# Performance work log

Measured on AMD Instinct MI355X. Metric: run time of the kernel, lower is better.

## Reference

```python
import jax, jax.numpy as jnp
import numpy as np

DIM = 512
NUM_HEADS = 8
HEAD_DIM = DIM // NUM_HEADS
MAX_SLICES = 1024
SCALE = float(np.sqrt(HEAD_DIM))


def setup_inputs() -> dict:
    key = jax.random.key(0)
    ks = jax.random.split(key, 12)
    B, Nv, Nt, D = 4, 1024, 512, DIM
    std = 0.02
    inp = {
        "visual_tokens": jax.random.normal(ks[0], (B, Nv, D), jnp.float32),
        "text_tokens": jax.random.normal(ks[1], (B, Nt, D), jnp.float32),
        # Linear weights stored as [in, out] (i.e., torch W^T), so y = x @ W + b
        "W_Q": jax.random.normal(ks[2], (D, D), jnp.float32) * std,
        "b_Q": jnp.zeros((D,), jnp.float32),
        "W_K": jax.random.normal(ks[3], (D, D), jnp.float32) * std,
        "b_K": jnp.zeros((D,), jnp.float32),
        "W_V": jax.random.normal(ks[4], (D, D), jnp.float32) * std,
        "b_V": jnp.zeros((D,), jnp.float32),
        "W_O": jax.random.normal(ks[5], (D, D), jnp.float32) * std,
        "b_O": jnp.zeros((D,), jnp.float32),
        "bias_table": jax.random.normal(ks[6], (2 * MAX_SLICES - 1, NUM_HEADS), jnp.float32) * std,
        "ln_gamma": jnp.ones((D,), jnp.float32),
        "ln_beta": jnp.zeros((D,), jnp.float32),
    }
    return inp


def _layernorm(x, gamma, beta, eps=1e-5):
    mu = jnp.mean(x, axis=-1, keepdims=True)
    var = jnp.var(x, axis=-1, keepdims=True)
    return (x - mu) * jax.lax.rsqrt(var + eps) * gamma + beta


def reference(visual_tokens, text_tokens, W_Q, b_Q, W_K, b_K, W_V, b_V, W_O, b_O,
              bias_table, ln_gamma, ln_beta):
    Z = jnp.concatenate([visual_tokens, text_tokens], axis=1)  # [B, N, D]
    B, N, D = Z.shape
    Z = _layernorm(Z, ln_gamma, ln_beta)

    def proj(W, b):
        return (Z @ W + b).reshape(B, N, NUM_HEADS, HEAD_DIM).transpose(0, 2, 1, 3)

    Q = proj(W_Q, b_Q)  # [B, H, N, hd]
    K = proj(W_K, b_K)
    V = proj(W_V, b_V)

    attn = jnp.einsum("bhqd,bhkd->bhqk", Q, K) / SCALE  # [B, H, N, N]

    # relative slice bias: [H, N, N]
    coords = jnp.arange(N)
    rel = coords[:, None] - coords[None, :] + (MAX_SLICES - 1)
    rel = jnp.clip(rel, 0, 2 * MAX_SLICES - 2)
    bias = bias_table[rel]                      # [N, N, H]
    bias = jnp.transpose(bias, (2, 0, 1))[None]  # [1, H, N, N]

    attn = jax.nn.softmax(attn + bias, axis=-1)
    out = jnp.einsum("bhqk,bhkd->bhqd", attn, V)  # [B, H, N, hd]
    out = out.transpose(0, 2, 1, 3).reshape(B, N, D)
    return out @ W_O + b_O
```

## Files before the change

kernel.cpp:

```cpp
#include <hip/hip_runtime.h>
#include <stdint.h>

#define NSEQ   1536
#define NBATCH 4
#define NM     (NBATCH * NSEQ)
#define DMODEL 512
#define NHEAD  8
#define HD     64
#define TBLN   2047

typedef __attribute__((ext_vector_type(4))) float  f32x4;
typedef __attribute__((ext_vector_type(4))) int    i32x4;
typedef __attribute__((ext_vector_type(8))) __bf16 bf16x8;
typedef unsigned short u16;

static_assert(sizeof(bf16x8) == 16, "bf16x8 must be 16B");

__device__ inline u16 f2bf(float f) {
  union { float f; uint32_t u; } v; v.f = f;
  uint32_t u = v.u;
  return (u16)((u + 0x7fffu + ((u >> 16) & 1u)) >> 16);
}

__device__ inline bf16x8 ld_bf8(const u16* p) {
  i32x4 v = *(const i32x4*)p;
  return __builtin_bit_cast(bf16x8, v);
}

__device__ inline f32x4 mfma16(bf16x8 a, bf16x8 b, f32x4 c) {
  return __builtin_amdgcn_mfma_f32_16x16x32_bf16(a, b, c, 0, 0, 0);
}

__device__ inline void gload_lds16(const void* g, void* l) {
  __builtin_amdgcn_global_load_lds(
      (__attribute__((address_space(1))) void*)(g),
      (__attribute__((address_space(3))) void*)(l), 16, 0, 0);
}

__device__ inline uint32_t pkbf(float a, float b) {
  uint32_t r;
  asm("v_cvt_pk_bf16_f32 %0, %1, %2" : "=v"(r) : "v"(a), "v"(b));
  return r;
}

__device__ inline float exp2_raw(float x) {
  float r;
  asm("v_exp_f32 %0, %1" : "=v"(r) : "v"(x));
  return r;
}

__global__ __launch_bounds__(256) void ln_kernel(
    const float* __restrict__ vis, const float* __restrict__ txt,
    const float* __restrict__ gamma, const float* __restrict__ beta,
    u16* __restrict__ zn) {
  const int lane = threadIdx.x & 63;
  const int row  = blockIdx.x * 4 + (threadIdx.x >> 6);
  const int b = row / NSEQ, n = row - b * NSEQ;
  const float* src = (n < 1024) ? (vis + ((size_t)b * 1024 + n) * DMODEL)
                                : (txt + ((size_t)b * 512 + (n - 1024)) * DMODEL);
  const float4* s4 = (const float4*)src;
  float4 x0 = s4[lane], x1 = s4[lane + 64];
  float s = x0.x + x0.y + x0.z + x0.w + x1.x + x1.y + x1.z + x1.w;
  float q = x0.x*x0.x + x0.y*x0.y + x0.z*x0.z + x0.w*x0.w
          + x1.x*x1.x + x1.y*x1.y + x1.z*x1.z + x1.w*x1.w;
  #pragma unroll
  for (int m = 1; m < 64; m <<= 1) { s += __shfl_xor(s, m); q += __shfl_xor(q, m); }
  const float mean = s * (1.0f / 512.0f);
  const float var  = q * (1.0f / 512.0f) - mean * mean;
  const float rstd = rsqrtf(var + 1e-5f);
  const float4* g4 = (const float4*)gamma;
  const float4* b4 = (const float4*)beta;
  float4 g0 = g4[lane], g1 = g4[lane + 64], p0 = b4[lane], p1 = b4[lane + 64];
  u16* dst = zn + (size_t)row * DMODEL;
  ushort4 o0, o1;
  o0.x = f2bf((x0.x - mean) * rstd * g0.x + p0.x);
  o0.y = f2bf((x0.y - mean) * rstd * g0.y + p0.y);
  o0.z = f2bf((x0.z - mean) * rstd * g0.z + p0.z);
  o0.w = f2bf((x0.w - mean) * rstd * g0.w + p0.w);
  o1.x = f2bf((x1.x - mean) * rstd * g1.x + p1.x);
  o1.y = f2bf((x1.y - mean) * rstd * g1.y + p1.y);
  o1.z = f2bf((x1.z - mean) * rstd * g1.z + p1.z);
  o1.w = f2bf((x1.w - mean) * rstd * g1.w + p1.w);
  *(ushort4*)(dst + lane * 4)        = o0;
  *(ushort4*)(dst + (lane + 64) * 4) = o1;
}

__global__ __launch_bounds__(256) void wtrans_kernel(
    const float* __restrict__ WQ, const float* __restrict__ WK,
    const float* __restrict__ WV, const float* __restrict__ WO,
    u16* __restrict__ wqkvt, u16* __restrict__ wot) {
  __shared__ float t[32][33];
  const int m = blockIdx.z;
  const float* W = (m == 0) ? WQ : (m == 1) ? WK : (m == 2) ? WV : WO;
  const int n0 = blockIdx.x * 32, k0 = blockIdx.y * 32;
  const int tx = threadIdx.x & 31, ty = threadIdx.x >> 5;
  #pragma unroll
  for (int j = 0; j < 4; ++j)
    t[ty + j * 8][tx] = W[(size_t)(k0 + ty + j * 8) * DMODEL + n0 + tx];
  __syncthreads();
  u16* out = (m < 3) ? (wqkvt + (size_t)m * DMODEL * DMODEL) : wot;
  #pragma unroll
  for (int j = 0; j < 4; ++j)
    out[(size_t)(n0 + ty + j * 8) * DMODEL + k0 + tx] = f2bf(t[tx][ty + j * 8]);
}

__global__ __launch_bounds__(256) void gemm_qkv(
    const u16* __restrict__ A, const u16* __restrict__ Bt,
    const float* __restrict__ bQ, const float* __restrict__ bK, const float* __restrict__ bV,
    u16* __restrict__ Q, u16* __restrict__ Kk, u16* __restrict__ Vt) {
  __shared__ __align__(16) u16 lat[128 * 64];
  __shared__ __align__(16) u16 lbt[96 * 64];
  const int tid = threadIdx.x, lane = tid & 63, w = tid >> 6;
  const int wr = w >> 1, wc = w & 1;
  const int m0 = blockIdx.y * 128, n0 = blockIdx.x * 96;
  f32x4 acc[4][3] = {};
  for (int kt = 0; kt < 8; ++kt) {
    const int k0 = kt * 64;
    #pragma unroll
    for (int i = 0; i < 4; ++i) {
      int ch = tid + 256 * i;
      int row = ch >> 3, pc = ch & 7;
      int kk = k0 + ((pc ^ (row & 7)) << 3);
      gload_lds16(A + (size_t)(m0 + row) * DMODEL + kk, lat + (size_t)ch * 8);
    }
    #pragma unroll
    for (int i = 0; i < 3; ++i) {
      int ch = tid + 256 * i;
      int row = ch >> 3, pc = ch & 7;
      int kk = k0 + ((pc ^ (row & 7)) << 3);
      gload_lds16(Bt + (size_t)(n0 + row) * DMODEL + kk, lbt + (size_t)ch * 8);
    }
    __syncthreads();
    #pragma unroll
    for (int ks = 0; ks < 2; ++ks) {
      bf16x8 af[4], bfr[3];
      const int cc = ks * 4 + (lane >> 4);
      #pragma unroll
      for (int f = 0; f < 4; ++f) {
        int ra = wr * 64 + f * 16 + (lane & 15);
        af[f]  = ld_bf8(lat + ra * 64 + ((cc ^ (ra & 7)) << 3));
      }
      #pragma unroll
      for (int f = 0; f < 3; ++f) {
        int rb = wc * 48 + f * 16 + (lane & 15);
        bfr[f] = ld_bf8(lbt + rb * 64 + ((cc ^ (rb & 7)) << 3));
      }
      #pragma unroll
      for (int fr = 0; fr < 4; ++fr)
        #pragma unroll
        for (int fc = 0; fc < 3; ++fc)
          acc[fr][fc] = mfma16(af[fr], bfr[fc], acc[fr][fc]);
    }
    __syncthreads();
  }
  #pragma unroll
  for (int fr = 0; fr < 4; ++fr) {
    const int mbase = m0 + wr * 64 + fr * 16 + ((lane >> 4) << 2);
    const int b = mbase / NSEQ;
    const int nseq = mbase - b * NSEQ;
    #pragma unroll
    for (int fc = 0; fc < 3; ++fc) {
      const int col = n0 + wc * 48 + fc * 16 + (lane & 15);
      const int which = col >> 9;
      const int cw = col & 511;
      const int h = cw >> 6, d = cw & 63;
      const float bias = (which == 0) ? bQ[cw] : (which == 1) ? bK[cw] : bV[cw];
      if (which < 2) {
        u16* dst = ((which == 0) ? Q : Kk) + ((size_t)(b * NHEAD + h) * NSEQ + nseq) * HD + d;
        #pragma unroll
        for (int r = 0; r < 4; ++r) dst[(size_t)r * HD] = f2bf(acc[fr][fc][r] + bias);
      } else {
        ushort4 pv;
        pv.x = f2bf(acc[fr][fc][0] + bias);
        pv.y = f2bf(acc[fr][fc][1] + bias);
        pv.z = f2bf(acc[fr][fc][2] + bias);
        pv.w = f2bf(acc[fr][fc][3] + bias);
        *(ushort4*)(Vt + ((size_t)(b * NHEAD + h) * HD + d) * NSEQ + nseq) = pv;
      }
    }
  }
}

__global__ __launch_bounds__(256) void gemm_oproj(
    const u16* __restrict__ A, const u16* __restrict__ Bt,
    const float* __restrict__ bO, float* __restrict__ out) {
  __shared__ __align__(16) u16 lat[64 * 64];
  __shared__ __align__(16) u16 lbt[64 * 64];
  const int tid = threadIdx.x, lane = tid & 63, w = tid >> 6;
  const int wr = w >> 1, wc = w & 1;
  const int m0 = blockIdx.y * 64, n0 = blockIdx.x * 64;
  f32x4 acc[2][2] = {};
  for (int kt = 0; kt < 8; ++kt) {
    const int k0 = kt * 64;
    #pragma unroll
    for (int i = 0; i < 2; ++i) {
      int ch = tid + 256 * i;
      int row = ch >> 3, pc = ch & 7;
      int kk = k0 + ((pc ^ (row & 7)) << 3);
      gload_lds16(A  + (size_t)(m0 + row) * DMODEL + kk, lat + (size_t)ch * 8);
      gload_lds16(Bt + (size_t)(n0 + row) * DMODEL + kk, lbt + (size_t)ch * 8);
    }
    __syncthreads();
    #pragma unroll
    for (int ks = 0; ks < 2; ++ks) {
      bf16x8 af[2], bfr[2];
      const int cc = ks * 4 + (lane >> 4);
      #pragma unroll
      for (int f = 0; f < 2; ++f) {
        int ra = wr * 32 + f * 16 + (lane & 15);
        af[f]  = ld_bf8(lat + ra * 64 + ((cc ^ (ra & 7)) << 3));
        int rb = wc * 32 + f * 16 + (lane & 15);
        bfr[f] = ld_bf8(lbt + rb * 64 + ((cc ^ (rb & 7)) << 3));
      }
      #pragma unroll
      for (int fr = 0; fr < 2; ++fr)
        #pragma unroll
        for (int fc = 0; fc < 2; ++fc)
          acc[fr][fc] = mfma16(af[fr], bfr[fc], acc[fr][fc]);
    }
    __syncthreads();
  }
  #pragma unroll
  for (int fr = 0; fr < 2; ++fr) {
    const int mbase = m0 + wr * 32 + fr * 16 + ((lane >> 4) << 2);
    #pragma unroll
    for (int fc = 0; fc < 2; ++fc) {
      const int col = n0 + wc * 32 + fc * 16 + (lane & 15);
      const float bias = bO[col];
      float* dst = out + (size_t)mbase * DMODEL + col;
      #pragma unroll
      for (int r = 0; r < 4; ++r) dst[(size_t)r * DMODEL] = acc[fr][fc][r] + bias;
    }
  }
}

__global__ __launch_bounds__(384, 2) void attn_kernel(
    const u16* __restrict__ Q, const u16* __restrict__ K,
    const u16* __restrict__ Vt, const float* __restrict__ table,
    u16* __restrict__ O) {
  __shared__ float rblds[3072];
  __shared__ __align__(16) u16 kbuf[2][8192];
  __shared__ __align__(16) u16 vbuf[2][8192];
  __shared__ __align__(16) u16 plds[6][4096];
  const int tid = threadIdx.x, lane = tid & 63, w = tid >> 6;
  const int bid = blockIdx.x;
  const int xcd = bid & 7, idx = bid >> 3;
  const int bh  = xcd * 4 + (idx & 3);
  const int qt  = idx >> 2;
  const int h   = bh & (NHEAD - 1);
  for (int t = tid; t < 3072; t += 384) {
    int src = 2558 - t;
    src = src < 0 ? 0 : (src > 2046 ? 2046 : src);
    rblds[t] = table[(size_t)src * NHEAD + h] * 1.4426950408889634f;
  }

  const int lo16 = lane & 15, g = lane >> 4;
  const int q0 = qt * 192 + w * 32;
  const u16* Qb = Q  + (size_t)bh * NSEQ * HD;
  const u16* Kb = K  + (size_t)bh * NSEQ * HD;
  const u16* Vb = Vt + (size_t)bh * HD * NSEQ;

#define STAGE2(buf, k0)                                                        \
  if (tid < 256) {                                                             \
    _Pragma("unroll")                                                          \
    for (int i = 0; i < 4; ++i) {                                              \
      int ch = tid + 256 * i;                                                  \
      int krow = ch >> 3;                                                      \
      int kcol = ((ch ^ krow) & 7) << 3;                                       \
      gload_lds16(Kb + (size_t)((k0) + krow) * HD + kcol, kbuf[buf] + (size_t)ch * 8); \
      int vrow = ch >> 4;                                                      \
      int vcg  = (ch & 8) | ((ch ^ vrow) & 7);                                 \
      gload_lds16(Vb + (size_t)vrow * NSEQ + (k0) + vcg * 8, vbuf[buf] + (size_t)ch * 8); \
    }                                                                          \
  }

  bf16x8 qf[2][2];
  #pragma unroll
  for (int s = 0; s < 2; ++s)
    #pragma unroll
    for (int kd = 0; kd < 2; ++kd)
      qf[s][kd] = ld_bf8(Qb + (size_t)(q0 + s * 16 + lo16) * HD + kd * 32 + g * 8);

  float l_part[2] = {0.f, 0.f};
  f32x4 acc[2][4] = {};

  char* plb = (char*)plds[w];
  const int pswz  = (lo16 & 7) << 4;
  const int wbase = lo16 * 128;
  const int rswz  = lo16 & 7;
  const float* rbp = rblds + (1535 - q0 - lo16 + 4 * g - 16);
  const float c1 = 0.125f * 1.4426950408889634f;

  STAGE2(0, 0);
  __syncthreads();
  int cur = 0;

  for (int kt = 0; kt < 12; ++kt) {
    const int k0 = kt * 128;
    const int nxt = cur ^ 1;
    if (kt < 11) {
      STAGE2(nxt, k0 + 128);
      if (tid < 256) asm volatile("s_waitcnt vmcnt(8)" ::: "memory");
    } else {
      if (tid < 256) asm volatile("s_waitcnt vmcnt(0)" ::: "memory");
    }
    __builtin_amdgcn_s_barrier();
    const u16* kb = kbuf[cur];
    const u16* vb = vbuf[cur];
    #pragma unroll
    for (int hh = 0; hh < 2; ++hh) {
      char* plh = plb + hh * 4096;
      float bvg[5][4];
      #pragma unroll
      for (int j = 0; j < 5; ++j)
        #pragma unroll
        for (int r = 0; r < 4; ++r)
          bvg[j][r] = rbp[k0 + hh * 64 + 16 * j + r];
      f32x4 st[2][4] = {};
      __builtin_amdgcn_s_setprio(1);
      #pragma unroll
      for (int kc = 0; kc < 4; ++kc) {
        const int row = hh * 64 + kc * 16 + lo16;
        const bf16x8 kf0 = ld_bf8(kb + row * 64 + ((g ^ rswz) << 3));
        const bf16x8 kf1 = ld_bf8(kb + row * 64 + (((4 + g) ^ rswz) << 3));
        #pragma unroll
        for (int s = 0; s < 2; ++s) {
          st[s][kc] = mfma16(kf0, qf[s][0], st[s][kc]);
          st[s][kc] = mfma16(kf1, qf[s][1], st[s][kc]);
        }
      }
      __builtin_amdgcn_s_setprio(0);
      #pragma unroll
      for (int s = 0; s < 2; ++s)
        #pragma unroll
        for (int kc = 0; kc < 4; ++kc) {
          #pragma unroll
          for (int r = 0; r < 4; ++r) {
            float p = exp2_raw(__builtin_fmaf(st[s][kc][r], c1, bvg[kc - s + 1][r]));
            st[s][kc][r] = p;
            l_part[s] += p;
          }
          uint2 pr;
          pr.x = pkbf(st[s][kc][0], st[s][kc][1]);
          pr.y = pkbf(st[s][kc][2], st[s][kc][3]);
          *(uint2*)(plh + s * 2048 + wbase + ((kc * 32 + g * 8) ^ pswz)) = pr;
        }
      __builtin_amdgcn_s_setprio(1);
      #pragma unroll
      for (int t = 0; t < 2; ++t) {
        bf16x8 pb[2];
        #pragma unroll
        for (int s = 0; s < 2; ++s)
          pb[s] = ld_bf8((const u16*)(plh + s * 2048 + wbase + ((t * 64 + g * 16) ^ pswz)));
        #pragma unroll
        for (int fc = 0; fc < 4; ++fc) {
          const int row = fc * 16 + lo16;
          const int cl = (hh * 8) | (((t * 4 + g) ^ rswz) & 7);
          const bf16x8 vf = ld_bf8(vb + row * 128 + cl * 8);
          #pragma unroll
          for (int s = 0; s < 2; ++s)
            acc[s][fc] = mfma16(vf, pb[s], acc[s][fc]);
        }
      }
      __builtin_amdgcn_s_setprio(0);
    }
    __builtin_amdgcn_s_barrier();
    cur = nxt;
  }
  const int b = bh >> 3;
  #pragma unroll
  for (int s = 0; s < 2; ++s) {
    float l_r = l_part[s];
    l_r += __shfl_xor(l_r, 16);
    l_r += __shfl_xor(l_r, 32);
    const float inv = 1.0f / l_r;
    u16* orow = O + ((size_t)(b * NSEQ + q0 + s * 16 + lo16)) * DMODEL + h * HD;
    #pragma unroll
    for (int fc = 0; fc < 4; ++fc) {
      uint2 o4;
      o4.x = pkbf(acc[s][fc][0] * inv, acc[s][fc][1] * inv);
      o4.y = pkbf(acc[s][fc][2] * inv, acc[s][fc][3] * inv);
      *(uint2*)(orow + fc * 16 + g * 4) = o4;
    }
  }
#undef STAGE2
}

extern "C" void kernel_launch(void* const* d_in, const int* in_sizes, int n_in,
                              void* d_out, int out_size, void* d_ws, size_t ws_size,
                              hipStream_t stream) {
  const float* vis   = (const float*)d_in[0];
  const float* txt   = (const float*)d_in[1];
  const float* WQ    = (const float*)d_in[2];
  const float* bQ    = (const float*)d_in[3];
  const float* WK    = (const float*)d_in[4];
  const float* bK    = (const float*)d_in[5];
  const float* WV    = (const float*)d_in[6];
  const float* bV    = (const float*)d_in[7];
  const float* WO    = (const float*)d_in[8];
  const float* bO    = (const float*)d_in[9];
  const float* table = (const float*)d_in[10];
  const float* gamma = (const float*)d_in[11];
  const float* beta  = (const float*)d_in[12];
  float* out = (float*)d_out;

  char* p = (char*)d_ws;
  u16* zn    = (u16*)p; p += (size_t)NM * DMODEL * 2;
  u16* wqkvt = (u16*)p; p += (size_t)3 * DMODEL * DMODEL * 2;
  u16* wot   = (u16*)p; p += (size_t)DMODEL * DMODEL * 2;
  u16* q     = (u16*)p; p += (size_t)NM * DMODEL * 2;
  u16* k     = (u16*)p; p += (size_t)NM * DMODEL * 2;
  u16* vt    = (u16*)p; p += (size_t)NM * DMODEL * 2;
  u16* o     = (u16*)p; p += (size_t)NM * DMODEL * 2;

  hipLaunchKernelGGL(ln_kernel, dim3(NM / 4), dim3(256), 0, stream,
                     vis, txt, gamma, beta, zn);
  hipLaunchKernelGGL(wtrans_kernel, dim3(16, 16, 4), dim3(256), 0, stream,
                     WQ, WK, WV, WO, wqkvt, wot);
  hipLaunchKernelGGL(gemm_qkv, dim3(16, 48), dim3(256), 0, stream,
                     zn, wqkvt, bQ, bK, bV, q, k, vt);
  hipLaunchKernelGGL(attn_kernel, dim3(256), dim3(384), 0, stream,
                     q, k, vt, table, o);
  hipLaunchKernelGGL(gemm_oproj, dim3(8, 96), dim3(256), 0, stream,
                     o, wot, bO, out);
}
```

Measured before the change: 85.01 us.

## Restructure attention to 4 waves with 48 query rows each and 64-key tiles

```diff
diff --git a/kernel.cpp b/kernel.cpp
--- a/kernel.cpp
+++ b/kernel.cpp
@@ -47,6 +47,13 @@
   float r;
   asm("v_exp_f32 %0, %1" : "=v"(r) : "v"(x));
   return r;
+}
+
+__device__ inline float bfhi(uint32_t u) {
+  union { uint32_t u; float f; } v; v.u = u & 0xffff0000u; return v.f;
+}
+__device__ inline float bflo(uint32_t u) {
+  union { uint32_t u; float f; } v; v.u = u << 16; return v.f;
 }
 
 __global__ __launch_bounds__(256) void ln_kernel(
@@ -234,142 +241,143 @@
   }
 }
 
-__global__ __launch_bounds__(384, 2) void attn_kernel(
+__global__ __launch_bounds__(256, 2) void attn_kernel(
     const u16* __restrict__ Q, const u16* __restrict__ K,
     const u16* __restrict__ Vt, const float* __restrict__ table,
     u16* __restrict__ O) {
-  __shared__ float rblds[3072];
-  __shared__ __align__(16) u16 kbuf[2][8192];
-  __shared__ __align__(16) u16 vbuf[2][8192];
-  __shared__ __align__(16) u16 plds[6][4096];
+  __shared__ u16 rb2[2][3072];
+  __shared__ __align__(16) u16 kbuf[2][4096];
+  __shared__ __align__(16) u16 vbuf[2][4096];
+  __shared__ __align__(16) u16 plds[4][3][1024];
   const int tid = threadIdx.x, lane = tid & 63, w = tid >> 6;
   const int bid = blockIdx.x;
   const int xcd = bid & 7, idx = bid >> 3;
   const int bh  = xcd * 4 + (idx & 3);
   const int qt  = idx >> 2;
   const int h   = bh & (NHEAD - 1);
-  for (int t = tid; t < 3072; t += 384) {
-    int src = 2558 - t;
+  for (int t = tid; t < 2 * 3072; t += 256) {
+    const int c = (t >= 3072) ? 1 : 0;
+    const int x = t - c * 3072;
+    int src = 2558 - (x + c);
     src = src < 0 ? 0 : (src > 2046 ? 2046 : src);
-    rblds[t] = table[(size_t)src * NHEAD + h] * 1.4426950408889634f;
+    rb2[c][x] = f2bf(table[(size_t)src * NHEAD + h] * 1.4426950408889634f);
   }
 
   const int lo16 = lane & 15, g = lane >> 4;
-  const int q0 = qt * 192 + w * 32;
+  const int q0 = qt * 192 + w * 48;
   const u16* Qb = Q  + (size_t)bh * NSEQ * HD;
   const u16* Kb = K  + (size_t)bh * NSEQ * HD;
   const u16* Vb = Vt + (size_t)bh * HD * NSEQ;
 
-#define STAGE2(buf, k0)                                                        \
-  if (tid < 256) {                                                             \
-    _Pragma("unroll")                                                          \
-    for (int i = 0; i < 4; ++i) {                                              \
-      int ch = tid + 256 * i;                                                  \
-      int krow = ch >> 3;                                                      \
-      int kcol = ((ch ^ krow) & 7) << 3;                                       \
-      gload_lds16(Kb + (size_t)((k0) + krow) * HD + kcol, kbuf[buf] + (size_t)ch * 8); \
-      int vrow = ch >> 4;                                                      \
-      int vcg  = (ch & 8) | ((ch ^ vrow) & 7);                                 \
-      gload_lds16(Vb + (size_t)vrow * NSEQ + (k0) + vcg * 8, vbuf[buf] + (size_t)ch * 8); \
-    }                                                                          \
-  }
-
-  bf16x8 qf[2][2];
-  #pragma unroll
-  for (int s = 0; s < 2; ++s)
+#define STAGE(buf, k0)                                                        \
+  do {                                                                        \
+    _Pragma("unroll")                                                         \
+    for (int i = 0; i < 2; ++i) {                                             \
+      int ch = tid + 256 * i;                                                 \
+      int row = ch >> 3, pc = ch & 7;                                         \
+      int col = (pc ^ (row & 7)) << 3;                                        \
+      gload_lds16(Kb + (size_t)((k0) + row) * HD + col, kbuf[buf] + (size_t)ch * 8); \
+      gload_lds16(Vb + (size_t)row * NSEQ + (k0) + col, vbuf[buf] + (size_t)ch * 8); \
+    }                                                                         \
+  } while (0)
+
+  bf16x8 qf[3][2];
+  #pragma unroll
+  for (int s = 0; s < 3; ++s)
     #pragma unroll
     for (int kd = 0; kd < 2; ++kd)
       qf[s][kd] = ld_bf8(Qb + (size_t)(q0 + s * 16 + lo16) * HD + kd * 32 + g * 8);
 
-  float l_part[2] = {0.f, 0.f};
-  f32x4 acc[2][4] = {};
-
-  char* plb = (char*)plds[w];
+  float l_part[3] = {0.f, 0.f, 0.f};
+  f32x4 acc[3][4] = {};
+
   const int pswz  = (lo16 & 7) << 4;
   const int wbase = lo16 * 128;
   const int rswz  = lo16 & 7;
-  const float* rbp = rblds + (1535 - q0 - lo16 + 4 * g - 16);
+  const int B   = 1535 - q0 - lo16 + 4 * g - 32;
+  const int c2  = B & 1;
+  const int dwb = (B - c2) >> 1;
+  const uint32_t* rbp32 = (const uint32_t*)rb2[c2];
   const float c1 = 0.125f * 1.4426950408889634f;
 
-  STAGE2(0, 0);
+  STAGE(0, 0);
   __syncthreads();
   int cur = 0;
 
-  for (int kt = 0; kt < 12; ++kt) {
-    const int k0 = kt * 128;
+  for (int kt = 0; kt < 24; ++kt) {
+    const int k0 = kt * 64;
     const int nxt = cur ^ 1;
-    if (kt < 11) {
-      STAGE2(nxt, k0 + 128);
-      if (tid < 256) asm volatile("s_waitcnt vmcnt(8)" ::: "memory");
+    if (kt < 23) {
+      STAGE(nxt, k0 + 64);
+      asm volatile("s_waitcnt vmcnt(4)" ::: "memory");
     } else {
-      if (tid < 256) asm volatile("s_waitcnt vmcnt(0)" ::: "memory");
+      asm volatile("s_waitcnt vmcnt(0)" ::: "memory");
     }
     __builtin_amdgcn_s_barrier();
     const u16* kb = kbuf[cur];
     const u16* vb = vbuf[cur];
-    #pragma unroll
-    for (int hh = 0; hh < 2; ++hh) {
-      char* plh = plb + hh * 4096;
-      float bvg[5][4];
-      #pragma unroll
-      for (int j = 0; j < 5; ++j)
+    float bvf[6][4];
+    #pragma unroll
+    for (int j = 0; j < 6; ++j) {
+      const uint32_t u0 = rbp32[dwb + (k0 >> 1) + 8 * j];
+      const uint32_t u1 = rbp32[dwb + (k0 >> 1) + 8 * j + 1];
+      bvf[j][0] = bflo(u0); bvf[j][1] = bfhi(u0);
+      bvf[j][2] = bflo(u1); bvf[j][3] = bfhi(u1);
+    }
+    f32x4 st[3][4] = {};
+    __builtin_amdgcn_s_setprio(1);
+    #pragma unroll
+    for (int kc = 0; kc < 4; ++kc) {
+      const int row = kc * 16 + lo16;
+      const bf16x8 kf0 = ld_bf8(kb + row * 64 + ((g ^ rswz) << 3));
+      const bf16x8 kf1 = ld_bf8(kb + row * 64 + (((4 + g) ^ rswz) << 3));
+      #pragma unroll
+      for (int s = 0; s < 3; ++s) {
+        st[s][kc] = mfma16(kf0, qf[s][0], st[s][kc]);
+        st[s][kc] = mfma16(kf1, qf[s][1], st[s][kc]);
+      }
+    }
+    __builtin_amdgcn_s_setprio(0);
+    #pragma unroll
+    for (int s = 0; s < 3; ++s) {
+      char* plb = (char*)plds[w][s];
+      #pragma unroll
+      for (int kc = 0; kc < 4; ++kc) {
         #pragma unroll
-        for (int r = 0; r < 4; ++r)
-          bvg[j][r] = rbp[k0 + hh * 64 + 16 * j + r];
-      f32x4 st[2][4] = {};
-      __builtin_amdgcn_s_setprio(1);
-      #pragma unroll
-      for (int kc = 0; kc < 4; ++kc) {
-        const int row = hh * 64 + kc * 16 + lo16;
-        const bf16x8 kf0 = ld_bf8(kb + row * 64 + ((g ^ rswz) << 3));
-        const bf16x8 kf1 = ld_bf8(kb + row * 64 + (((4 + g) ^ rswz) << 3));
+        for (int r = 0; r < 4; ++r) {
+          float p = exp2_raw(__builtin_fmaf(st[s][kc][r], c1, bvf[kc - s + 2][r]));
+          st[s][kc][r] = p;
+          l_part[s] += p;
+        }
+        uint2 pr;
+        pr.x = pkbf(st[s][kc][0], st[s][kc][1]);
+        pr.y = pkbf(st[s][kc][2], st[s][kc][3]);
+        *(uint2*)(plb + wbase + ((kc * 32 + g * 8) ^ pswz)) = pr;
+      }
+    }
+    __builtin_amdgcn_s_setprio(1);
+    #pragma unroll
+    for (int t = 0; t < 2; ++t) {
+      bf16x8 pb[3];
+      #pragma unroll
+      for (int s = 0; s < 3; ++s)
+        pb[s] = ld_bf8((const u16*)((char*)plds[w][s] + wbase + ((t * 64 + g * 16) ^ pswz)));
+      #pragma unroll
+      for (int fc = 0; fc < 4; ++fc) {
+        const int row = fc * 16 + lo16;
+        const bf16x8 vf = ld_bf8(vb + row * 64 + (((t * 4 + g) ^ rswz) << 3));
         #pragma unroll
-        for (int s = 0; s < 2; ++s) {
-          st[s][kc] = mfma16(kf0, qf[s][0], st[s][kc]);
-          st[s][kc] = mfma16(kf1, qf[s][1], st[s][kc]);
-        }
-      }
-      __builtin_amdgcn_s_setprio(0);
-      #pragma unroll
-      for (int s = 0; s < 2; ++s)
-        #pragma unroll
-        for (int kc = 0; kc < 4; ++kc) {
-          #pragma unroll
-          for (int r = 0; r < 4; ++r) {
-            float p = exp2_raw(__builtin_fmaf(st[s][kc][r], c1, bvg[kc - s + 1][r]));
-            st[s][kc][r] = p;
-            l_part[s] += p;
-          }
-          uint2 pr;
-          pr.x = pkbf(st[s][kc][0], st[s][kc][1]);
-          pr.y = pkbf(st[s][kc][2], st[s][kc][3]);
-          *(uint2*)(plh + s * 2048 + wbase + ((kc * 32 + g * 8) ^ pswz)) = pr;
-        }
-      __builtin_amdgcn_s_setprio(1);
-      #pragma unroll
-      for (int t = 0; t < 2; ++t) {
-        bf16x8 pb[2];
-        #pragma unroll
-        for (int s = 0; s < 2; ++s)
-          pb[s] = ld_bf8((const u16*)(plh + s * 2048 + wbase + ((t * 64 + g * 16) ^ pswz)));
-        #pragma unroll
-        for (int fc = 0; fc < 4; ++fc) {
-          const int row = fc * 16 + lo16;
-          const int cl = (hh * 8) | (((t * 4 + g) ^ rswz) & 7);
-          const bf16x8 vf = ld_bf8(vb + row * 128 + cl * 8);
-          #pragma unroll
-          for (int s = 0; s < 2; ++s)
-            acc[s][fc] = mfma16(vf, pb[s], acc[s][fc]);
-        }
-      }
-      __builtin_amdgcn_s_setprio(0);
-    }
+        for (int s = 0; s < 3; ++s)
+          acc[s][fc] = mfma16(vf, pb[s], acc[s][fc]);
+      }
+    }
+    __builtin_amdgcn_s_setprio(0);
     __builtin_amdgcn_s_barrier();
     cur = nxt;
   }
   const int b = bh >> 3;
   #pragma unroll
-  for (int s = 0; s < 2; ++s) {
+  for (int s = 0; s < 3; ++s) {
     float l_r = l_part[s];
     l_r += __shfl_xor(l_r, 16);
     l_r += __shfl_xor(l_r, 32);
@@ -383,7 +391,7 @@
       *(uint2*)(orow + fc * 16 + g * 4) = o4;
     }
   }
-#undef STAGE2
+#undef STAGE
 }
 
 extern "C" void kernel_launch(void* const* d_in, const int* in_sizes, int n_in,
@@ -419,7 +427,7 @@
                      WQ, WK, WV, WO, wqkvt, wot);
   hipLaunchKernelGGL(gemm_qkv, dim3(16, 48), dim3(256), 0, stream,
                      zn, wqkvt, bQ, bK, bV, q, k, vt);
-  hipLaunchKernelGGL(attn_kernel, dim3(256), dim3(384), 0, stream,
+  hipLaunchKernelGGL(attn_kernel, dim3(256), dim3(256), 0, stream,
                      q, k, vt, table, o);
   hipLaunchKernelGGL(gemm_oproj, dim3(8, 96), dim3(256), 0, stream,
                      o, wot, bO, out);
```

After: 91.02 us. 1.07x slower.
